# Kernel optimization log

Hardware: AMD Instinct MI355X
Metric: run time of the kernel (lower is better)

The kernel has to match this reference:

```python
import jax, jax.numpy as jnp
import numpy as np

SIZES = [(200000, 100000), (100000, 50000), (50000, 25000)]  # (n_src, n_dst) per layer
E = [1600000, 800000, 400000]
IN_C, HID, OUT_C = 128, 256, 47
BN_EPS = 1e-5


def setup_inputs() -> dict:
    key = jax.random.key(0)
    ks = jax.random.split(key, 32)
    inp = {"x": jax.random.normal(ks[0], (SIZES[0][0], IN_C), jnp.float32)}
    for i in range(3):
        inp[f"row{i}"] = jax.random.randint(ks[1 + 2 * i], (E[i],), 0, SIZES[i][0], dtype=jnp.int32)
        inp[f"col{i}"] = jax.random.randint(ks[2 + 2 * i], (E[i],), 0, SIZES[i][1], dtype=jnp.int32)
    dims = [IN_C, HID, HID]
    for i in range(3):
        inp[f"Wl{i}"] = jax.random.normal(ks[10 + 4 * i], (HID, dims[i]), jnp.float32) * 0.05
        inp[f"Wr{i}"] = jax.random.normal(ks[11 + 4 * i], (HID, dims[i]), jnp.float32) * 0.05
        inp[f"g{i}"] = jnp.ones((HID,), jnp.float32)
        inp[f"b{i}"] = jnp.zeros((HID,), jnp.float32)
    inp["Wlin"] = jax.random.normal(ks[25], (OUT_C, 3 * HID), jnp.float32) * 0.05
    inp["blin"] = jnp.zeros((OUT_C,), jnp.float32)
    return inp


def _sage_bn_relu(x_src, row, col, Wl, Wr, g, b, n_dst):
    """Bipartite SAGEConv (mean aggr, bias=False) + BatchNorm(eval) + ReLU."""
    x_dst = x_src[:n_dst]
    msg = x_src[row]                                             # [E, d] gather
    agg = jax.ops.segment_sum(msg, col, num_segments=n_dst)      # scatter-add
    cnt = jax.ops.segment_sum(jnp.ones(row.shape, x_src.dtype), col, num_segments=n_dst)
    agg = agg / jnp.maximum(cnt, 1.0)[:, None]                   # mean over in-neighbors
    h = agg @ Wl.T + x_dst @ Wr.T                                # lin_l + lin_r
    # BatchNorm1d in eval mode with fresh running stats (mean=0, var=1)
    h = h * jax.lax.rsqrt(jnp.asarray(1.0 + BN_EPS, h.dtype)) * g + b
    return jax.nn.relu(h)


def reference(x, row0, col0, row1, col1, row2, col2,
              Wl0, Wr0, g0, b0, Wl1, Wr1, g1, b1, Wl2, Wr2, g2, b2,
              Wlin, blin):
    rows = (row0, row1, row2)
    cols = (col0, col1, col2)
    Wls, Wrs = (Wl0, Wl1, Wl2), (Wr0, Wr1, Wr2)
    gs, bs = (g0, g1, g2), (b0, b1, b2)
    end = SIZES[-1][1]  # end_size = adj_t[-1][-1][1]
    h = x
    xs = []
    for i in range(3):
        h = _sage_bn_relu(h, rows[i], cols[i], Wls[i], Wrs[i], gs[i], bs[i], SIZES[i][1])
        xs.append(h[:end])
    z = jnp.concatenate(xs, axis=-1) @ Wlin.T + blin  # JK 'cat' + final Linear
    return jax.nn.log_softmax(z, axis=-1)
```

## Files before the change

### kernel.cpp

```cpp
#include <hip/hip_runtime.h>
#include <hip/hip_bf16.h>


#define N_DST0 100000
#define N_DST1 50000
#define N_DST2 25000
#define HID 256
#define OUTC 47
#define ENDR 25000
#define DRC 512
#define NBMAX 256
#define CHUNK 8192
#define BN_SCALE 0.99999500003749969f

#define SEL3(y, a, b, c) ((y) == 0 ? (a) : ((y) == 1 ? (b) : (c)))

typedef _Float16 f16x8 __attribute__((ext_vector_type(8)));
typedef _Float16 f16x4 __attribute__((ext_vector_type(4)));
typedef __attribute__((ext_vector_type(4))) float f32x4;

__device__ __forceinline__ f16x8 hshfl_add(f16x8 a, int m) {
    union { f16x8 h; int i[4]; } u, v;
    u.h = a;
#pragma unroll
    for (int j = 0; j < 4; ++j) v.i[j] = __shfl_xor(u.i[j], m);
    return a + v.h;
}

__global__ __launch_bounds__(256) void f2h_kernel(
    const float* __restrict__ in, _Float16* __restrict__ out, int n)
{
    int i = (blockIdx.x * 256 + threadIdx.x) * 4;
    if (i < n) {
        float4 v = *(const float4*)&in[i];
        f16x4 o = {(_Float16)v.x, (_Float16)v.y, (_Float16)v.z, (_Float16)v.w};
        *(f16x4*)&out[i] = o;
    }
}

__global__ __launch_bounds__(256) void f2h_multi(
    const float* s0, const float* s1, const float* s2, const float* s3,
    const float* s4, const float* s5, const float* s6,
    _Float16* d0, _Float16* d1, _Float16* d2, _Float16* d3,
    _Float16* d4, _Float16* d5, _Float16* d6)
{
    int idx = (blockIdx.x * 256 + threadIdx.x) * 4;
    const float* s; _Float16* d; int off;
    if (idx < 65536)       { if (idx < 32768)  { s = s0; d = d0; off = 0; }
                             else              { s = s1; d = d1; off = 32768; } }
    else if (idx < 196608) { if (idx < 131072) { s = s2; d = d2; off = 65536; }
                             else              { s = s3; d = d3; off = 131072; } }
    else if (idx < 327680) { if (idx < 262144) { s = s4; d = d4; off = 196608; }
                             else              { s = s5; d = d5; off = 262144; } }
    else if (idx < 363776) { s = s6; d = d6; off = 327680; }
    else return;
    int j = idx - off;
    float4 v = *(const float4*)&s[j];
    f16x4 o = {(_Float16)v.x, (_Float16)v.y, (_Float16)v.z, (_Float16)v.w};
    *(f16x4*)&d[j] = o;
}

__global__ __launch_bounds__(256) void bucket_hist_all(
    const int* c0, const int* c1, const int* c2,
    int* __restrict__ bhist, int E0, int E1, int E2)
{
    const int y = blockIdx.y;
    const int* col = SEL3(y, c0, c1, c2);
    const int E = SEL3(y, E0, E1, E2);
    __shared__ int h[NBMAX];
    const int t = threadIdx.x;
    h[t] = 0;
    __syncthreads();
    const int stride = gridDim.x * 256;
    for (int i = blockIdx.x * 256 + t; i < E; i += stride)
        atomicAdd(&h[col[i] >> 9], 1);
    __syncthreads();
    int v = h[t];
    if (v) atomicAdd(&bhist[(y * NBMAX + t) * 16], v);
}

__global__ __launch_bounds__(256) void bucket_scan_all(
    const int* __restrict__ bhist, int* __restrict__ bstart,
    int* __restrict__ bcur)
{
    const int y = blockIdx.x;
    const int t = threadIdx.x;
    __shared__ int sh[256];
    int v = bhist[(y * NBMAX + t) * 16];
    sh[t] = v;
    __syncthreads();
    for (int off = 1; off < 256; off <<= 1) {
        int x = (t >= off) ? sh[t - off] : 0;
        __syncthreads();
        sh[t] += x;
        __syncthreads();
    }
    int ex = sh[t] - v;
    bstart[y * (NBMAX + 1) + t] = ex;
    if (t == 255) bstart[y * (NBMAX + 1) + 256] = sh[255];
    bcur[y * NBMAX * 16 + t * 16] = ex;
}

__global__ __launch_bounds__(256) void multisplit_all(
    const int* r0, const int* r1, const int* r2,
    const int* c0, const int* c1, const int* c2,
    int* bcur, unsigned int* p0, unsigned int* p1, unsigned int* p2,
    int E0, int E1, int E2)
{
    const int y = blockIdx.y;
    const int E = SEL3(y, E0, E1, E2);
    const int base = blockIdx.x * CHUNK;
    if (base >= E) return;
    const int* row = SEL3(y, r0, r1, r2);
    const int* col = SEL3(y, c0, c1, c2);
    int* bc = bcur + y * (NBMAX * 16);
    unsigned int* part = SEL3(y, p0, p1, p2);

    __shared__ int hist[NBMAX];
    __shared__ int segoff[NBMAX + 1];
    __shared__ int cur[NBMAX];
    __shared__ int delta[NBMAX];
    __shared__ unsigned int stage[CHUNK];
    __shared__ unsigned char bstage[CHUNK];

    const int t = threadIdx.x;
    const int n = min(CHUNK, E - base);

    hist[t] = 0;
    __syncthreads();
    for (int i = t; i < n; i += 256)
        atomicAdd(&hist[col[base + i] >> 9], 1);
    __syncthreads();

    int v = hist[t];
    cur[t] = v;
    __syncthreads();
    for (int off = 1; off < 256; off <<= 1) {
        int x = (t >= off) ? cur[t - off] : 0;
        __syncthreads();
        cur[t] += x;
        __syncthreads();
    }
    segoff[t + 1] = cur[t];
    if (t == 0) segoff[0] = 0;
    __syncthreads();
    int so = segoff[t];
    cur[t] = so;
    if (v > 0) {
        int g = atomicAdd(&bc[t * 16], v);
        delta[t] = g - so;
    }
    __syncthreads();

    for (int i = t; i < n; i += 256) {
        int c = col[base + i];
        int r = row[base + i];
        int b = c >> 9;
        int p = atomicAdd(&cur[b], 1);
        stage[p] = ((unsigned)(c & 511) << 18) | (unsigned)r;
        bstage[p] = (unsigned char)b;
    }
    __syncthreads();

    for (int i = t; i < n; i += 256) {
        int b = bstage[i];
        part[delta[b] + i] = stage[i];
    }
}

__global__ __launch_bounds__(256) void bucket_csr_all(
    const unsigned int* p0, const unsigned int* p1, const unsigned int* p2,
    const int* __restrict__ bstart,
    int* g0, int* g1, int* g2, int* x0, int* x1, int* x2,
    int* s0, int* s1, int* s2, int n0, int n1, int n2)
{
    const int y = blockIdx.y;
    const int n_dst = SEL3(y, n0, n1, n2);
    const int b = blockIdx.x;
    const int d0 = b * DRC;
    if (d0 >= n_dst) return;
    const unsigned int* part = SEL3(y, p0, p1, p2);
    const int* bs = bstart + y * (NBMAX + 1);
    int* deg  = SEL3(y, g0, g1, g2);
    int* excl = SEL3(y, x0, x1, x2);
    int* esrc = SEL3(y, s0, s1, s2);

    __shared__ int h[DRC];
    __shared__ int cur2[DRC];
    __shared__ int tsum[256];
    const int t = threadIdx.x;
    h[t] = 0; h[t + 256] = 0;
    __syncthreads();
    const int wstart = bs[b], wend = bs[b + 1];
    for (int i = wstart + t; i < wend; i += 256)
        atomicAdd(&h[part[i] >> 18], 1);
    __syncthreads();

    int h0 = h[2 * t], h1 = h[2 * t + 1];
    int ps = h0 + h1;
    tsum[t] = ps;
    __syncthreads();
    for (int off = 1; off < 256; off <<= 1) {
        int x = (t >= off) ? tsum[t - off] : 0;
        __syncthreads();
        tsum[t] += x;
        __syncthreads();
    }
    int exp_ = tsum[t] - ps;
    cur2[2 * t]     = wstart + exp_;
    cur2[2 * t + 1] = wstart + exp_ + h0;
    __syncthreads();

    for (int j = t; j < DRC; j += 256) {
        int d = d0 + j;
        if (d < n_dst) { deg[d] = h[j]; excl[d] = cur2[j]; }
    }
    __syncthreads();

    for (int i = wstart + t; i < wend; i += 256) {
        unsigned int v = part[i];
        int pos = atomicAdd(&cur2[v >> 18], 1);
        esrc[pos] = (int)(v & 0x3FFFFu);
    }
}

template<int LOGK>
__global__ __launch_bounds__(256) void gather_mean(
    const _Float16* __restrict__ xsrc, const int* __restrict__ esrc,
    const int* __restrict__ start, const int* __restrict__ deg,
    _Float16* __restrict__ agg, int n_dst)
{
    const int wid = (blockIdx.x * 256 + threadIdx.x) >> 6;
    const int lane = threadIdx.x & 63;
    if (wid >= n_dst) return;
    const int s = start[wid];
    const int d = deg[wid];
    const float inv = 1.0f / (float)max(d, 1);
    f16x8 acc = {0, 0, 0, 0, 0, 0, 0, 0};

    if (LOGK == 7) {
        const int sub = lane >> 4;
        const int cl  = lane & 15;
        const size_t coff = (size_t)cl * 8;
        int i = 0;
        for (; i + 8 <= d; i += 8) {
            int e0 = esrc[s + i + sub], e1 = esrc[s + i + 4 + sub];
            f16x8 v0 = *(const f16x8*)&xsrc[((size_t)e0 << 7) + coff];
            f16x8 v1 = *(const f16x8*)&xsrc[((size_t)e1 << 7) + coff];
            acc += v0;
            acc += v1;
        }
        for (; i + 4 <= d; i += 4) {
            int e0 = esrc[s + i + sub];
            acc += *(const f16x8*)&xsrc[((size_t)e0 << 7) + coff];
        }
        if (i + sub < d) {
            int e0 = esrc[s + i + sub];
            acc += *(const f16x8*)&xsrc[((size_t)e0 << 7) + coff];
        }
        acc = hshfl_add(acc, 16);
        acc = hshfl_add(acc, 32);
        if (sub == 0) {
            f16x8 o;
#pragma unroll
            for (int j = 0; j < 8; ++j) o[j] = (_Float16)((float)acc[j] * inv);
            *(f16x8*)&agg[((size_t)wid << 7) + coff] = o;
        }
    } else {
        const int sub = lane >> 5;
        const int cl  = lane & 31;
        const size_t coff = (size_t)cl * 8;
        int i = 0;
        for (; i + 8 <= d; i += 8) {
            int e0 = esrc[s + i + sub],     e1 = esrc[s + i + 2 + sub];
            int e2 = esrc[s + i + 4 + sub], e3 = esrc[s + i + 6 + sub];
            f16x8 v0 = *(const f16x8*)&xsrc[((size_t)e0 << 8) + coff];
            f16x8 v1 = *(const f16x8*)&xsrc[((size_t)e1 << 8) + coff];
            f16x8 v2 = *(const f16x8*)&xsrc[((size_t)e2 << 8) + coff];
            f16x8 v3 = *(const f16x8*)&xsrc[((size_t)e3 << 8) + coff];
            acc += v0; acc += v1; acc += v2; acc += v3;
        }
        for (; i + 2 <= d; i += 2) {
            int e0 = esrc[s + i + sub];
            acc += *(const f16x8*)&xsrc[((size_t)e0 << 8) + coff];
        }
        if (i + sub < d) {
            int e0 = esrc[s + i + sub];
            acc += *(const f16x8*)&xsrc[((size_t)e0 << 8) + coff];
        }
        acc = hshfl_add(acc, 32);
        if (sub == 0) {
            f16x8 o;
#pragma unroll
            for (int j = 0; j < 8; ++j) o[j] = (_Float16)((float)acc[j] * inv);
            *(f16x8*)&agg[((size_t)wid << 8) + coff] = o;
        }
    }
}

template<int KH>
__global__ __launch_bounds__(512) void sage_gemm_mfma(
    const _Float16* __restrict__ aggb, const _Float16* __restrict__ xdstb,
    const _Float16* __restrict__ Wlb, const _Float16* __restrict__ Wrb,
    const float* __restrict__ g, const float* __restrict__ b,
    _Float16* __restrict__ h, int n_dst)
{
    __shared__ uint4 SH[2176];
    uint4* A_sh = SH;
    uint4* B_sh = SH + 512;

    const int tid  = threadIdx.x;
    const int lane = tid & 63;
    const int wv   = tid >> 6;
    const int mh   = wv >> 2;
    const int n0   = (wv & 3) * 64;
    const int m0g  = blockIdx.x * 128;
    const int lrow = lane & 15;
    const int lgrp = lane >> 4;

    f32x4 acc[4][4];
#pragma unroll
    for (int i = 0; i < 4; ++i)
#pragma unroll
        for (int j = 0; j < 4; ++j)
            acc[i][j] = (f32x4){0.f, 0.f, 0.f, 0.f};

    for (int kp = 0; kp < 2 * KH; kp += 32) {
        const _Float16* Asrc = (kp < KH) ? aggb : xdstb;
        const _Float16* Bsrc = (kp < KH) ? Wlb : Wrb;
        const int kbase = (kp < KH) ? kp : kp - KH;

        {
            int m = tid >> 2, gq = tid & 3;
            int r = m0g + m;
            uint4 v = {0, 0, 0, 0};
            if (r < n_dst) v = *(const uint4*)&Asrc[(size_t)r * KH + kbase + gq * 8];
            A_sh[m * 4 + (gq ^ ((m >> 1) & 3))] = v;
        }
        {
            int nb_ = tid >> 2, gq = tid & 3;
#pragma unroll
            for (int i2 = 0; i2 < 2; ++i2) {
                int n = nb_ + 128 * i2;
                uint4 v = *(const uint4*)&Bsrc[(size_t)n * KH + kbase + gq * 8];
                B_sh[n * 4 + (gq ^ ((n >> 1) & 3))] = v;
            }
        }
        __syncthreads();

        f16x8 av[4], bv[4];
#pragma unroll
        for (int mf = 0; mf < 4; ++mf) {
            int m = mh * 64 + mf * 16 + lrow;
            av[mf] = *reinterpret_cast<const f16x8*>(&A_sh[m * 4 + (lgrp ^ ((m >> 1) & 3))]);
        }
#pragma unroll
        for (int nf = 0; nf < 4; ++nf) {
            int n = n0 + nf * 16 + lrow;
            bv[nf] = *reinterpret_cast<const f16x8*>(&B_sh[n * 4 + (lgrp ^ ((n >> 1) & 3))]);
        }
#pragma unroll
        for (int mf = 0; mf < 4; ++mf)
#pragma unroll
            for (int nf = 0; nf < 4; ++nf)
                acc[mf][nf] = __builtin_amdgcn_mfma_f32_16x16x32_f16(
                    av[mf], bv[nf], acc[mf][nf], 0, 0, 0);
        __syncthreads();
    }

    unsigned short* C_sh = (unsigned short*)SH;
#pragma unroll
    for (int half = 0; half < 2; ++half) {
        __syncthreads();
        if (mh == half) {
#pragma unroll
            for (int nf = 0; nf < 4; ++nf) {
                int n = n0 + nf * 16 + lrow;
                float sc = g[n] * BN_SCALE;
                float bi = b[n];
#pragma unroll
                for (int mf = 0; mf < 4; ++mf) {
                    int mloc = mf * 16 + lgrp * 4;
#pragma unroll
                    for (int r = 0; r < 4; ++r) {
                        float vv = fmaxf(acc[mf][nf][r] * sc + bi, 0.f);
                        _Float16 hv = (_Float16)vv;
                        C_sh[(mloc + r) * 264 + n] = *(unsigned short*)&hv;
                    }
                }
            }
        }
        __syncthreads();
        int mbase = m0g + half * 64;
#pragma unroll
        for (int k = 0; k < 4; ++k) {
            int idx = tid + k * 512;
            int rr = idx >> 5, cc = idx & 31;
            int m = mbase + rr;
            if (m < n_dst)
                *(uint4*)&h[(size_t)m * HID + cc * 8] =
                    *(const uint4*)&C_sh[rr * 264 + cc * 8];
        }
    }
}

__global__ __launch_bounds__(256) void final_mfma(
    const _Float16* __restrict__ h0, const _Float16* __restrict__ h1,
    const _Float16* __restrict__ h2, const _Float16* __restrict__ wlinb,
    const float* __restrict__ blin, float* __restrict__ out)
{
    __shared__ uint4 A_sh[512];
    __shared__ uint4 B_sh[256];

    const int tid  = threadIdx.x;
    const int lane = tid & 63;
    const int wv   = tid >> 6;
    const int m0g  = blockIdx.x * 128;
    const int lrow = lane & 15;
    const int lgrp = lane >> 4;

    f32x4 acc[2][4];
#pragma unroll
    for (int i = 0; i < 2; ++i)
#pragma unroll
        for (int j = 0; j < 4; ++j)
            acc[i][j] = (f32x4){0.f, 0.f, 0.f, 0.f};

    for (int kp = 0; kp < 768; kp += 32) {
        const int seg = kp >> 8;
        const _Float16* hs = (seg == 0) ? h0 : (seg == 1) ? h1 : h2;
        const int kseg = kp & 255;

#pragma unroll
        for (int l = 0; l < 2; ++l) {
            int idx = tid + l * 256;
            int m = idx >> 2, gq = idx & 3;
            int r = m0g + m;
            uint4 v = {0, 0, 0, 0};
            if (r < ENDR) v = *(const uint4*)&hs[(size_t)r * HID + kseg + gq * 8];
            A_sh[m * 4 + (gq ^ ((m >> 1) & 3))] = v;
        }
        {
            int n = tid >> 2, gq = tid & 3;
            uint4 v = *(const uint4*)&wlinb[(size_t)n * 768 + kp + gq * 8];
            B_sh[n * 4 + (gq ^ ((n >> 1) & 3))] = v;
        }
        __syncthreads();

        f16x8 av[2], bv[4];
#pragma unroll
        for (int mf = 0; mf < 2; ++mf) {
            int m = wv * 32 + mf * 16 + lrow;
            av[mf] = *reinterpret_cast<const f16x8*>(&A_sh[m * 4 + (lgrp ^ ((m >> 1) & 3))]);
        }
#pragma unroll
        for (int nf = 0; nf < 4; ++nf) {
            int n = nf * 16 + lrow;
            bv[nf] = *reinterpret_cast<const f16x8*>(&B_sh[n * 4 + (lgrp ^ ((n >> 1) & 3))]);
        }
#pragma unroll
        for (int mf = 0; mf < 2; ++mf)
#pragma unroll
            for (int nf = 0; nf < 4; ++nf)
                acc[mf][nf] = __builtin_amdgcn_mfma_f32_16x16x32_f16(
                    av[mf], bv[nf], acc[mf][nf], 0, 0, 0);
        __syncthreads();
    }

    float bv4[4];
#pragma unroll
    for (int nf = 0; nf < 4; ++nf) {
        int n = nf * 16 + lrow;
        bv4[nf] = (n < OUTC) ? blin[n] : 0.f;
    }

#pragma unroll
    for (int mf = 0; mf < 2; ++mf) {
        float z[4][4];
        float rmax[4], rsum[4];
#pragma unroll
        for (int r = 0; r < 4; ++r) {
            float mx = -INFINITY;
#pragma unroll
            for (int nf = 0; nf < 4; ++nf) {
                int n = nf * 16 + lrow;
                float v = (n < OUTC) ? acc[mf][nf][r] + bv4[nf] : -INFINITY;
                z[r][nf] = v;
                mx = fmaxf(mx, v);
            }
            rmax[r] = mx;
        }
#pragma unroll
        for (int off = 8; off >= 1; off >>= 1)
#pragma unroll
            for (int r = 0; r < 4; ++r)
                rmax[r] = fmaxf(rmax[r], __shfl_xor(rmax[r], off));
#pragma unroll
        for (int r = 0; r < 4; ++r) {
            float s = 0.f;
#pragma unroll
            for (int nf = 0; nf < 4; ++nf)
                s += (z[r][nf] > -INFINITY) ? expf(z[r][nf] - rmax[r]) : 0.f;
            rsum[r] = s;
        }
#pragma unroll
        for (int off = 8; off >= 1; off >>= 1)
#pragma unroll
            for (int r = 0; r < 4; ++r)
                rsum[r] += __shfl_xor(rsum[r], off);

#pragma unroll
        for (int r = 0; r < 4; ++r) {
            int m = m0g + wv * 32 + mf * 16 + lgrp * 4 + r;
            if (m < ENDR) {
                float lg = rmax[r] + logf(rsum[r]);
#pragma unroll
                for (int nf = 0; nf < 4; ++nf) {
                    int n = nf * 16 + lrow;
                    if (n < OUTC) out[(size_t)m * OUTC + n] = z[r][nf] - lg;
                }
            }
        }
    }
}

extern "C" void kernel_launch(void* const* d_in, const int* in_sizes, int n_in,
                              void* d_out, int out_size, void* d_ws, size_t ws_size,
                              hipStream_t stream)
{
    const float* x    = (const float*)d_in[0];
    const int* rows[3] = {(const int*)d_in[1], (const int*)d_in[3], (const int*)d_in[5]};
    const int* cols[3] = {(const int*)d_in[2], (const int*)d_in[4], (const int*)d_in[6]};
    const float* Wl[3] = {(const float*)d_in[7],  (const float*)d_in[11], (const float*)d_in[15]};
    const float* Wr[3] = {(const float*)d_in[8],  (const float*)d_in[12], (const float*)d_in[16]};
    const float* gs[3] = {(const float*)d_in[9],  (const float*)d_in[13], (const float*)d_in[17]};
    const float* bs[3] = {(const float*)d_in[10], (const float*)d_in[14], (const float*)d_in[18]};
    const float* Wlin = (const float*)d_in[19];
    const float* blin = (const float*)d_in[20];
    float* out = (float*)d_out;

    const int E0 = in_sizes[1], E1 = in_sizes[3], E2 = in_sizes[5];

    char* base = (char*)d_ws;
    _Float16* xb   = (_Float16*)(base);
    _Float16* h0b  = (_Float16*)(base + 51200000);
    _Float16* h1b  = (_Float16*)(base + 102400000);
    _Float16* h2b  = (_Float16*)(base + 128000000);
    _Float16* aggb = (_Float16*)(base + 140800000);
    _Float16* wb   = (_Float16*)(base + 166400000);
    _Float16* wlinb= (_Float16*)(base + 167100032);
    int* ibase = (int*)(base + 167600000);
    int* esrc0 = ibase;
    int* esrc1 = ibase + 1600000;
    int* esrc2 = ibase + 2400000;
    int* deg0  = ibase + 2800000;
    int* deg1  = ibase + 2900000;
    int* deg2  = ibase + 2950000;
    int* excl0 = ibase + 3000000;
    int* excl1 = ibase + 3100000;
    int* excl2 = ibase + 3150000;
    int* bcur  = ibase + 3200000;
    int* bhist = ibase + 3220000;
    int* bstart= ibase + 3240000;
    unsigned int* part0 = (unsigned int*)(base + 181000000);
    unsigned int* part1 = (unsigned int*)(base + 188000000);
    unsigned int* part2 = (unsigned int*)(base + 192000000);

    _Float16* Wlb[3] = {wb,          wb + 65536,  wb + 196608};
    _Float16* Wrb[3] = {wb + 32768,  wb + 131072, wb + 262144};

    f2h_kernel<<<(25600000 / 4 + 255) / 256, 256, 0, stream>>>(x, xb, 25600000);
    hipMemsetAsync(wlinb, 0, 64 * 768 * sizeof(_Float16), stream);
    f2h_multi<<<356, 256, 0, stream>>>(
        Wl[0], Wr[0], Wl[1], Wr[1], Wl[2], Wr[2], Wlin,
        Wlb[0], Wrb[0], Wlb[1], Wrb[1], Wlb[2], Wrb[2], wlinb);

    hipMemsetAsync(bhist, 0, 3 * NBMAX * 16 * sizeof(int), stream);
    {
        dim3 gh(128, 3);
        bucket_hist_all<<<gh, 256, 0, stream>>>(
            cols[0], cols[1], cols[2], bhist, E0, E1, E2);
        bucket_scan_all<<<3, 256, 0, stream>>>(bhist, bstart, bcur);
        dim3 gms((E0 + CHUNK - 1) / CHUNK, 3);
        multisplit_all<<<gms, 256, 0, stream>>>(
            rows[0], rows[1], rows[2], cols[0], cols[1], cols[2],
            bcur, part0, part1, part2, E0, E1, E2);
        dim3 gbc((N_DST0 + DRC - 1) / DRC, 3);
        bucket_csr_all<<<gbc, 256, 0, stream>>>(
            part0, part1, part2, bstart,
            deg0, deg1, deg2, excl0, excl1, excl2,
            esrc0, esrc1, esrc2, N_DST0, N_DST1, N_DST2);
    }

    const _Float16* hsrc[3] = {xb, h0b, h1b};
    _Float16* hdst[3] = {h0b, h1b, h2b};
    int* esrcs[3] = {esrc0, esrc1, esrc2};
    int* excls[3] = {excl0, excl1, excl2};
    int* degs[3]  = {deg0, deg1, deg2};
    const int ndst[3] = {N_DST0, N_DST1, N_DST2};

    for (int L = 0; L < 3; ++L) {
        const int nd = ndst[L];
        if (L == 0) {
            gather_mean<7><<<(nd + 3) / 4, 256, 0, stream>>>(
                hsrc[L], esrcs[L], excls[L], degs[L], aggb, nd);
            sage_gemm_mfma<128><<<(nd + 127) / 128, 512, 0, stream>>>(
                aggb, hsrc[L], Wlb[L], Wrb[L], gs[L], bs[L], hdst[L], nd);
        } else {
            gather_mean<8><<<(nd + 3) / 4, 256, 0, stream>>>(
                hsrc[L], esrcs[L], excls[L], degs[L], aggb, nd);
            sage_gemm_mfma<256><<<(nd + 127) / 128, 512, 0, stream>>>(
                aggb, hsrc[L], Wlb[L], Wrb[L], gs[L], bs[L], hdst[L], nd);
        }
    }

    final_mfma<<<(ENDR + 127) / 128, 256, 0, stream>>>(
        h0b, h1b, h2b, wlinb, blin, out);
}
```

Before: 372.9 us.

## Fuse neighbor mean-gather into SAGE MFMA GEMM via shared-memory aggregate tile

Replaces the separate gather_mean and sage_gemm kernels with one fused kernel per layer. Each block first gathers and averages the neighbor features for its tile of destination rows into LDS, then runs the MFMA GEMM reading the left operand from LDS. This removes the global round trip of the aggregated features and one launch per layer. Layers 1 and 2 use 64-row tiles with 8 waves along N. The Wlin padding memset is folded into the conversion kernel. The cost is that gather latency is no longer overlapped across kernels and each block holds a larger LDS footprint, which may lower occupancy.

```diff
diff --git a/kernel.cpp b/kernel.cpp
--- a/kernel.cpp
+++ b/kernel.cpp
@@ -19,6 +19,8 @@
 typedef _Float16 f16x4 __attribute__((ext_vector_type(4)));
 typedef __attribute__((ext_vector_type(4))) float f32x4;
 
+union U4H8 { uint4 u; f16x8 h; };
+
 __device__ __forceinline__ f16x8 hshfl_add(f16x8 a, int m) {
     union { f16x8 h; int i[4]; } u, v;
     u.h = a;
@@ -53,6 +55,12 @@
     else if (idx < 327680) { if (idx < 262144) { s = s4; d = d4; off = 196608; }
                              else              { s = s5; d = d5; off = 262144; } }
     else if (idx < 363776) { s = s6; d = d6; off = 327680; }
+    else if (idx < 393216) {
+        int j = idx - 327680;
+        f16x4 z = {0, 0, 0, 0};
+        *(f16x4*)&d6[j] = z;
+        return;
+    }
     else return;
     int j = idx - off;
     float4 v = *(const float4*)&s[j];
@@ -224,119 +232,98 @@
     }
 }
 
-template<int LOGK>
-__global__ __launch_bounds__(256) void gather_mean(
-    const _Float16* __restrict__ xsrc, const int* __restrict__ esrc,
-    const int* __restrict__ start, const int* __restrict__ deg,
-    _Float16* __restrict__ agg, int n_dst)
-{
-    const int wid = (blockIdx.x * 256 + threadIdx.x) >> 6;
-    const int lane = threadIdx.x & 63;
-    if (wid >= n_dst) return;
-    const int s = start[wid];
-    const int d = deg[wid];
-    const float inv = 1.0f / (float)max(d, 1);
-    f16x8 acc = {0, 0, 0, 0, 0, 0, 0, 0};
-
-    if (LOGK == 7) {
-        const int sub = lane >> 4;
-        const int cl  = lane & 15;
-        const size_t coff = (size_t)cl * 8;
-        int i = 0;
-        for (; i + 8 <= d; i += 8) {
-            int e0 = esrc[s + i + sub], e1 = esrc[s + i + 4 + sub];
-            f16x8 v0 = *(const f16x8*)&xsrc[((size_t)e0 << 7) + coff];
-            f16x8 v1 = *(const f16x8*)&xsrc[((size_t)e1 << 7) + coff];
-            acc += v0;
-            acc += v1;
-        }
-        for (; i + 4 <= d; i += 4) {
-            int e0 = esrc[s + i + sub];
-            acc += *(const f16x8*)&xsrc[((size_t)e0 << 7) + coff];
-        }
-        if (i + sub < d) {
-            int e0 = esrc[s + i + sub];
-            acc += *(const f16x8*)&xsrc[((size_t)e0 << 7) + coff];
-        }
-        acc = hshfl_add(acc, 16);
-        acc = hshfl_add(acc, 32);
-        if (sub == 0) {
-            f16x8 o;
-#pragma unroll
-            for (int j = 0; j < 8; ++j) o[j] = (_Float16)((float)acc[j] * inv);
-            *(f16x8*)&agg[((size_t)wid << 7) + coff] = o;
-        }
-    } else {
-        const int sub = lane >> 5;
-        const int cl  = lane & 31;
-        const size_t coff = (size_t)cl * 8;
-        int i = 0;
-        for (; i + 8 <= d; i += 8) {
-            int e0 = esrc[s + i + sub],     e1 = esrc[s + i + 2 + sub];
-            int e2 = esrc[s + i + 4 + sub], e3 = esrc[s + i + 6 + sub];
-            f16x8 v0 = *(const f16x8*)&xsrc[((size_t)e0 << 8) + coff];
-            f16x8 v1 = *(const f16x8*)&xsrc[((size_t)e1 << 8) + coff];
-            f16x8 v2 = *(const f16x8*)&xsrc[((size_t)e2 << 8) + coff];
-            f16x8 v3 = *(const f16x8*)&xsrc[((size_t)e3 << 8) + coff];
-            acc += v0; acc += v1; acc += v2; acc += v3;
-        }
-        for (; i + 2 <= d; i += 2) {
-            int e0 = esrc[s + i + sub];
-            acc += *(const f16x8*)&xsrc[((size_t)e0 << 8) + coff];
-        }
-        if (i + sub < d) {
-            int e0 = esrc[s + i + sub];
-            acc += *(const f16x8*)&xsrc[((size_t)e0 << 8) + coff];
-        }
-        acc = hshfl_add(acc, 32);
-        if (sub == 0) {
-            f16x8 o;
-#pragma unroll
-            for (int j = 0; j < 8; ++j) o[j] = (_Float16)((float)acc[j] * inv);
-            *(f16x8*)&agg[((size_t)wid << 8) + coff] = o;
-        }
-    }
-}
-
-template<int KH>
-__global__ __launch_bounds__(512) void sage_gemm_mfma(
-    const _Float16* __restrict__ aggb, const _Float16* __restrict__ xdstb,
+template<int KH, int TM>
+__global__ __launch_bounds__(512) void fused_sage(
+    const _Float16* __restrict__ xfeat,
+    const int* __restrict__ esrc, const int* __restrict__ excl,
+    const int* __restrict__ deg,
     const _Float16* __restrict__ Wlb, const _Float16* __restrict__ Wrb,
     const float* __restrict__ g, const float* __restrict__ b,
     _Float16* __restrict__ h, int n_dst)
 {
-    __shared__ uint4 SH[2176];
-    uint4* A_sh = SH;
-    uint4* B_sh = SH + 512;
+    constexpr int G    = KH / 8;
+    constexpr int NWN  = (TM == 128) ? 4 : 8;
+    constexpr int NPW  = 256 / NWN;
+    constexpr int NF   = NPW / 16;
+    constexpr int AGGU = TM * G;
+    constexpr int SUBS = (KH == 128) ? 4 : 2;
+    constexpr int RL   = 64 / SUBS;
+    constexpr int DPW  = TM / 8;
+
+    __shared__ uint4 SH[AGGU + 1024 + TM * 4];
+    uint4* Agg_sh = SH;
+    uint4* B_sh   = SH + AGGU;
+    uint4* Axd_sh = SH + AGGU + 1024;
 
     const int tid  = threadIdx.x;
     const int lane = tid & 63;
     const int wv   = tid >> 6;
-    const int mh   = wv >> 2;
-    const int n0   = (wv & 3) * 64;
-    const int m0g  = blockIdx.x * 128;
+    const int m0g  = blockIdx.x * TM;
+
+    {
+        const int sub = lane / RL;
+        const int cl  = lane % RL;
+        const size_t coff = (size_t)cl * 8;
+        int sj = 0, dj = 0;
+        {
+            int m = m0g + wv * DPW + lane;
+            if (lane < DPW && m < n_dst) { sj = excl[m]; dj = deg[m]; }
+        }
+        for (int j = 0; j < DPW; ++j) {
+            int s = __shfl(sj, j);
+            int d = __shfl(dj, j);
+            f16x8 acc = {0, 0, 0, 0, 0, 0, 0, 0};
+            int i = 0;
+            for (; i + 4 * SUBS <= d; i += 4 * SUBS) {
+                int e0 = esrc[s + i + sub];
+                int e1 = esrc[s + i + SUBS + sub];
+                int e2 = esrc[s + i + 2 * SUBS + sub];
+                int e3 = esrc[s + i + 3 * SUBS + sub];
+                f16x8 v0 = *(const f16x8*)&xfeat[((size_t)e0 << (KH == 128 ? 7 : 8)) + coff];
+                f16x8 v1 = *(const f16x8*)&xfeat[((size_t)e1 << (KH == 128 ? 7 : 8)) + coff];
+                f16x8 v2 = *(const f16x8*)&xfeat[((size_t)e2 << (KH == 128 ? 7 : 8)) + coff];
+                f16x8 v3 = *(const f16x8*)&xfeat[((size_t)e3 << (KH == 128 ? 7 : 8)) + coff];
+                acc += v0; acc += v1; acc += v2; acc += v3;
+            }
+            for (; i + SUBS <= d; i += SUBS) {
+                int e0 = esrc[s + i + sub];
+                acc += *(const f16x8*)&xfeat[((size_t)e0 << (KH == 128 ? 7 : 8)) + coff];
+            }
+            if (i + sub < d) {
+                int e0 = esrc[s + i + sub];
+                acc += *(const f16x8*)&xfeat[((size_t)e0 << (KH == 128 ? 7 : 8)) + coff];
+            }
+            if (KH == 128) { acc = hshfl_add(acc, 16); acc = hshfl_add(acc, 32); }
+            else           { acc = hshfl_add(acc, 32); }
+            if (sub == 0) {
+                float inv = 1.0f / (float)max(d, 1);
+                U4H8 o;
+#pragma unroll
+                for (int q = 0; q < 8; ++q) o.h[q] = (_Float16)((float)acc[q] * inv);
+                int mloc = wv * DPW + j;
+                Agg_sh[mloc * G + (cl & ~3) + ((cl & 3) ^ ((mloc >> 1) & 3))] = o.u;
+            }
+        }
+    }
+    __syncthreads();
+
     const int lrow = lane & 15;
     const int lgrp = lane >> 4;
-
-    f32x4 acc[4][4];
+    const int mh   = wv / NWN;
+    const int n0   = (wv % NWN) * NPW;
+
+    f32x4 acc2[4][NF];
 #pragma unroll
     for (int i = 0; i < 4; ++i)
 #pragma unroll
-        for (int j = 0; j < 4; ++j)
-            acc[i][j] = (f32x4){0.f, 0.f, 0.f, 0.f};
+        for (int j = 0; j < NF; ++j)
+            acc2[i][j] = (f32x4){0.f, 0.f, 0.f, 0.f};
 
     for (int kp = 0; kp < 2 * KH; kp += 32) {
-        const _Float16* Asrc = (kp < KH) ? aggb : xdstb;
-        const _Float16* Bsrc = (kp < KH) ? Wlb : Wrb;
-        const int kbase = (kp < KH) ? kp : kp - KH;
-
-        {
-            int m = tid >> 2, gq = tid & 3;
-            int r = m0g + m;
-            uint4 v = {0, 0, 0, 0};
-            if (r < n_dst) v = *(const uint4*)&Asrc[(size_t)r * KH + kbase + gq * 8];
-            A_sh[m * 4 + (gq ^ ((m >> 1) & 3))] = v;
-        }
+        const bool left = kp < KH;
+        const _Float16* Bsrc = left ? Wlb : Wrb;
+        const int kbase = left ? kp : kp - KH;
+
         {
             int nb_ = tid >> 2, gq = tid & 3;
 #pragma unroll
@@ -346,35 +333,51 @@
                 B_sh[n * 4 + (gq ^ ((n >> 1) & 3))] = v;
             }
         }
-        __syncthreads();
-
-        f16x8 av[4], bv[4];
+        if (!left) {
+            for (int idx = tid; idx < TM * 4; idx += 512) {
+                int m = idx >> 2, gq = idx & 3;
+                int r = m0g + m;
+                uint4 v = {0, 0, 0, 0};
+                if (r < n_dst) v = *(const uint4*)&xfeat[(size_t)r * KH + kbase + gq * 8];
+                Axd_sh[m * 4 + (gq ^ ((m >> 1) & 3))] = v;
+            }
+        }
+        __syncthreads();
+
+        f16x8 av[4], bv[NF];
+        const int kb4 = (kbase >> 3) & ~3;
 #pragma unroll
         for (int mf = 0; mf < 4; ++mf) {
             int m = mh * 64 + mf * 16 + lrow;
-            av[mf] = *reinterpret_cast<const f16x8*>(&A_sh[m * 4 + (lgrp ^ ((m >> 1) & 3))]);
-        }
-#pragma unroll
-        for (int nf = 0; nf < 4; ++nf) {
+            if (left)
+                av[mf] = *reinterpret_cast<const f16x8*>(
+                    &Agg_sh[m * G + kb4 + (lgrp ^ ((m >> 1) & 3))]);
+            else
+                av[mf] = *reinterpret_cast<const f16x8*>(
+                    &Axd_sh[m * 4 + (lgrp ^ ((m >> 1) & 3))]);
+        }
+#pragma unroll
+        for (int nf = 0; nf < NF; ++nf) {
             int n = n0 + nf * 16 + lrow;
             bv[nf] = *reinterpret_cast<const f16x8*>(&B_sh[n * 4 + (lgrp ^ ((n >> 1) & 3))]);
         }
 #pragma unroll
         for (int mf = 0; mf < 4; ++mf)
 #pragma unroll
-            for (int nf = 0; nf < 4; ++nf)
-                acc[mf][nf] = __builtin_amdgcn_mfma_f32_16x16x32_f16(
-                    av[mf], bv[nf], acc[mf][nf], 0, 0, 0);
+            for (int nf = 0; nf < NF; ++nf)
+                acc2[mf][nf] = __builtin_amdgcn_mfma_f32_16x16x32_f16(
+                    av[mf], bv[nf], acc2[mf][nf], 0, 0, 0);
         __syncthreads();
     }
 
     unsigned short* C_sh = (unsigned short*)SH;
-#pragma unroll
-    for (int half = 0; half < 2; ++half) {
+    constexpr int HALVES = TM / 64;
+#pragma unroll
+    for (int half = 0; half < HALVES; ++half) {
         __syncthreads();
         if (mh == half) {
 #pragma unroll
-            for (int nf = 0; nf < 4; ++nf) {
+            for (int nf = 0; nf < NF; ++nf) {
                 int n = n0 + nf * 16 + lrow;
                 float sc = g[n] * BN_SCALE;
                 float bi = b[n];
@@ -383,7 +386,7 @@
                     int mloc = mf * 16 + lgrp * 4;
 #pragma unroll
                     for (int r = 0; r < 4; ++r) {
-                        float vv = fmaxf(acc[mf][nf][r] * sc + bi, 0.f);
+                        float vv = fmaxf(acc2[mf][nf][r] * sc + bi, 0.f);
                         _Float16 hv = (_Float16)vv;
                         C_sh[(mloc + r) * 264 + n] = *(unsigned short*)&hv;
                     }
@@ -392,9 +395,7 @@
         }
         __syncthreads();
         int mbase = m0g + half * 64;
-#pragma unroll
-        for (int k = 0; k < 4; ++k) {
-            int idx = tid + k * 512;
+        for (int idx = tid; idx < 2048; idx += 512) {
             int rr = idx >> 5, cc = idx & 31;
             int m = mbase + rr;
             if (m < n_dst)
@@ -546,7 +547,6 @@
     _Float16* h0b  = (_Float16*)(base + 51200000);
     _Float16* h1b  = (_Float16*)(base + 102400000);
     _Float16* h2b  = (_Float16*)(base + 128000000);
-    _Float16* aggb = (_Float16*)(base + 140800000);
     _Float16* wb   = (_Float16*)(base + 166400000);
     _Float16* wlinb= (_Float16*)(base + 167100032);
     int* ibase = (int*)(base + 167600000);
@@ -570,8 +570,7 @@
     _Float16* Wrb[3] = {wb + 32768,  wb + 131072, wb + 262144};
 
     f2h_kernel<<<(25600000 / 4 + 255) / 256, 256, 0, stream>>>(x, xb, 25600000);
-    hipMemsetAsync(wlinb, 0, 64 * 768 * sizeof(_Float16), stream);
-    f2h_multi<<<356, 256, 0, stream>>>(
+    f2h_multi<<<384, 256, 0, stream>>>(
         Wl[0], Wr[0], Wl[1], Wr[1], Wl[2], Wr[2], Wlin,
         Wlb[0], Wrb[0], Wlb[1], Wrb[1], Wlb[2], Wrb[2], wlinb);
 
@@ -592,27 +591,12 @@
             esrc0, esrc1, esrc2, N_DST0, N_DST1, N_DST2);
     }
 
-    const _Float16* hsrc[3] = {xb, h0b, h1b};
-    _Float16* hdst[3] = {h0b, h1b, h2b};
-    int* esrcs[3] = {esrc0, esrc1, esrc2};
-    int* excls[3] = {excl0, excl1, excl2};
-    int* degs[3]  = {deg0, deg1, deg2};
-    const int ndst[3] = {N_DST0, N_DST1, N_DST2};
-
-    for (int L = 0; L < 3; ++L) {
-        const int nd = ndst[L];
-        if (L == 0) {
-            gather_mean<7><<<(nd + 3) / 4, 256, 0, stream>>>(
-                hsrc[L], esrcs[L], excls[L], degs[L], aggb, nd);
-            sage_gemm_mfma<128><<<(nd + 127) / 128, 512, 0, stream>>>(
-                aggb, hsrc[L], Wlb[L], Wrb[L], gs[L], bs[L], hdst[L], nd);
-        } else {
-            gather_mean<8><<<(nd + 3) / 4, 256, 0, stream>>>(
-                hsrc[L], esrcs[L], excls[L], degs[L], aggb, nd);
-            sage_gemm_mfma<256><<<(nd + 127) / 128, 512, 0, stream>>>(
-                aggb, hsrc[L], Wlb[L], Wrb[L], gs[L], bs[L], hdst[L], nd);
-        }
-    }
+    fused_sage<128, 128><<<(N_DST0 + 127) / 128, 512, 0, stream>>>(
+        xb, esrc0, excl0, deg0, Wlb[0], Wrb[0], gs[0], bs[0], h0b, N_DST0);
+    fused_sage<256, 64><<<(N_DST1 + 63) / 64, 512, 0, stream>>>(
+        h0b, esrc1, excl1, deg1, Wlb[1], Wrb[1], gs[1], bs[1], h1b, N_DST1);
+    fused_sage<256, 64><<<(N_DST2 + 63) / 64, 512, 0, stream>>>(
+        h1b, esrc2, excl2, deg2, Wlb[2], Wrb[2], gs[2], bs[2], h2b, N_DST2);
 
     final_mfma<<<(ENDR + 127) / 128, 256, 0, stream>>>(
         h0b, h1b, h2b, wlinb, blin, out);
```

Result: no change. 379.3 us (+1.7%).
